# Kernel optimization log

Measured on AMD Instinct MI355X. Metric: run time of the kernel, lower is better.

The kernel has to match this reference:

```python
import jax, jax.numpy as jnp
import numpy as np

H, E, V, F, P, B = 512, 512, 10000, 1280, 196, 32
SOS = 1

def setup_inputs() -> dict:
    key = jax.random.key(0)
    ks = jax.random.split(key, 24)
    s = 0.02
    return {
        "feature_outputs": jax.random.normal(ks[0], (B, P, F), jnp.float32),
        "caption": jax.random.randint(ks[1], (B, 80), 0, V),
        "max_caption": 80,
        "embedding": jax.random.normal(ks[2], (V, E), jnp.float32) * s,
        "W1_w": jax.random.normal(ks[3], (H, H), jnp.float32) * s,
        "W1_b": jnp.full((H,), 0.01, jnp.float32),
        "W2_w": jax.random.normal(ks[4], (H, F), jnp.float32) * s,
        "W2_b": jnp.full((H,), 0.01, jnp.float32),
        "Va_w": jax.random.normal(ks[5], (1, H), jnp.float32) * s,
        "Va_b": jnp.full((1,), 0.01, jnp.float32),
        "lstm_Wih": jax.random.normal(ks[6], (4 * H, E + F), jnp.float32) * s,
        "lstm_Whh": jax.random.normal(ks[7], (4 * H, H), jnp.float32) * s,
        "lstm_bih": jnp.zeros((4 * H,), jnp.float32),
        "lstm_bhh": jnp.zeros((4 * H,), jnp.float32),
        "out_w": jax.random.normal(ks[8], (V, H), jnp.float32) * s,
        "out_b": jnp.full((V,), 0.01, jnp.float32),
        "init_h_w": jax.random.normal(ks[9], (H, F), jnp.float32) * s,
        "init_h_b": jnp.full((H,), 0.01, jnp.float32),
        "init_c_w": jax.random.normal(ks[10], (H, F), jnp.float32) * s,
        "init_c_b": jnp.full((H,), 0.01, jnp.float32),
        "gate_w": jax.random.normal(ks[11], (F, H), jnp.float32) * s,
        "gate_b": jnp.full((F,), 0.01, jnp.float32),
    }


def reference(feature_outputs, caption, max_caption, embedding,
              W1_w, W1_b, W2_w, W2_b, Va_w, Va_b,
              lstm_Wih, lstm_Whh, lstm_bih, lstm_bhh,
              out_w, out_b, init_h_w, init_h_b, init_c_w, init_c_b,
              gate_w, gate_b):
    steps = int(max_caption)
    bsz = caption.shape[0]
    mean_enc = feature_outputs.mean(axis=1)                       # [B,F]
    h0 = mean_enc @ init_h_w.T + init_h_b                         # [B,H]
    c0 = mean_enc @ init_c_w.T + init_c_b                         # [B,H]
    # W2(keys) is constant across steps -> hoist out of the loop
    enc_proj = jnp.einsum('bpf,hf->bph', feature_outputs, W2_w) + W2_b  # [B,P,H]
    inp0 = jnp.broadcast_to(embedding[SOS], (bsz, embedding.shape[1]))  # [B,E]

    def step(carry, _):
        h, c, inp = carry
        # Bahdanau attention
        hid = h @ W1_w.T + W1_b                                   # [B,H]
        scores = (jax.nn.relu(hid[:, None, :] + enc_proj) @ Va_w[0] + Va_b[0])  # [B,P]
        weights = jax.nn.softmax(scores, axis=1)
        context = jnp.einsum('bpf,bp->bf', feature_outputs, weights)  # [B,F]
        gate = jax.nn.sigmoid(h @ gate_w.T + gate_b)              # [B,F]
        context = context * gate
        # LSTMCell (torch gate order: i, f, g, o)
        x = jnp.concatenate([inp, context], axis=1)               # [B,E+F]
        gates = x @ lstm_Wih.T + lstm_bih + h @ lstm_Whh.T + lstm_bhh
        i_g, f_g, g_g, o_g = jnp.split(gates, 4, axis=1)
        c_new = jax.nn.sigmoid(f_g) * c + jax.nn.sigmoid(i_g) * jnp.tanh(g_g)
        h_new = jax.nn.sigmoid(o_g) * jnp.tanh(c_new)
        logits = h_new @ out_w.T + out_b                          # [B,V] (dropout = eval identity)
        nxt = embedding[jnp.argmax(logits, axis=-1)]              # greedy decode
        return (h_new, c_new, nxt), (logits, weights)

    (h, c, _), (outs, attns) = jax.lax.scan(step, (h0, c0, inp0), None, length=steps)
    decoder_outputs = jnp.transpose(outs, (1, 0, 2))              # [B,T,V]
    attentions = jnp.transpose(attns, (1, 0, 2))                  # [B,T,P]
    return decoder_outputs, (h, c), attentions
```

## Files before the change

kernel.cpp:

```cpp
#include <hip/hip_runtime.h>
#include <hip/hip_cooperative_groups.h>
#include <math.h>

#define RI __restrict__

namespace {

constexpr int Hn=512, En=512, Vn=10000, Fn=1280, Pn=196, Bn=32, Tn=80;
constexpr int G4 = 2048, KX = 1792;
constexpr int NCAT = 13888;
constexpr int NVT = 157;
constexpr int J_GATE = 512, J_XP = 1792, J_LOG = 3840;
constexpr int NBLK = 256;

constexpr long O_ENC  = 0;
constexpr long O_W2T  = O_ENC  + (long)Bn*Pn*Hn;
constexpr long O_WCAT = O_W2T  + (long)Fn*Hn;
constexpr long O_WIHT = O_WCAT + (long)Hn*NCAT;
constexpr long O_H    = O_WIHT + (long)KX*G4;
constexpr long O_HT   = O_H    + (long)Bn*Hn;
constexpr long O_C    = O_HT   + (long)Hn*Bn;
constexpr long O_HID  = O_C    + (long)Bn*Hn;
constexpr long O_GT   = O_HID  + (long)Bn*Hn;
constexpr long O_XPT  = O_GT   + (long)Bn*Fn;
constexpr long O_XT   = O_XPT  + (long)G4*Bn;
constexpr long O_PMV  = O_XT   + (long)Bn*KX;
constexpr long O_PMI  = O_PMV  + (long)Bn*NVT;
constexpr long O_SVAL = O_PMI  + (long)Bn*NVT;
constexpr long O_SEL  = O_SVAL + (long)Bn*Pn;
constexpr long O_CNT  = O_SEL  + 64;
constexpr long O_IHCT  = O_ENC;
constexpr long O_MEANT = O_ENC + (long)Fn*1024;

__device__ __forceinline__ float sigm(float x){ return 1.0f/(1.0f+expf(-x)); }
__device__ __forceinline__ void fma4(float4& a, const float4 x, const float w){
  a.x += w*x.x; a.y += w*x.y; a.z += w*x.z; a.w += w*x.w;
}
__device__ __forceinline__ float ldc(const float* p){
  return __hip_atomic_load(p, __ATOMIC_RELAXED, __HIP_MEMORY_SCOPE_AGENT);
}
__device__ __forceinline__ void stc(float* p, float v){
  __hip_atomic_store(p, v, __ATOMIC_RELAXED, __HIP_MEMORY_SCOPE_AGENT);
}
__device__ __forceinline__ int ldci(const int* p){
  return __hip_atomic_load(p, __ATOMIC_RELAXED, __HIP_MEMORY_SCOPE_AGENT);
}
__device__ __forceinline__ void stci(int* p, int v){
  __hip_atomic_store(p, v, __ATOMIC_RELAXED, __HIP_MEMORY_SCOPE_AGENT);
}
__device__ __forceinline__ float2 ldc2(const float* p){
  union { unsigned long long u; float2 f; } c;
  c.u = __hip_atomic_load((const unsigned long long*)p,
                          __ATOMIC_RELAXED, __HIP_MEMORY_SCOPE_AGENT);
  return c.f;
}

__device__ __forceinline__ void gbar(unsigned* cnt, unsigned target){
  __syncthreads();
  if (threadIdx.x == 0){
    __hip_atomic_fetch_add(cnt, 1u, __ATOMIC_RELAXED, __HIP_MEMORY_SCOPE_AGENT);
    while (__hip_atomic_load(cnt, __ATOMIC_RELAXED, __HIP_MEMORY_SCOPE_AGENT) < target)
      __builtin_amdgcn_s_sleep(2);
  }
  __syncthreads();
}

__global__ __launch_bounds__(256) void k_tr_s(const float* RI src, float* RI dst,
                                              int R, int C, int S){
  __shared__ float t[32][33];
  int tc0 = blockIdx.x*32, tr0 = blockIdx.y*32;
  int lx = threadIdx.x & 31, ly = threadIdx.x >> 5;
  for (int i = ly; i < 32; i += 8){
    int r = tr0 + i, c = tc0 + lx;
    t[i][lx] = (r < R && c < C) ? src[(long)r*C + c] : 0.f;
  }
  __syncthreads();
  for (int i = ly; i < 32; i += 8){
    int c = tc0 + i, r = tr0 + lx;
    if (c < C && r < R) dst[(long)c*S + r] = t[lx][i];
  }
}

__global__ __launch_bounds__(256) void k_tr_wih(const float* RI src, float* RI ws){
  __shared__ float t[32][33];
  int tk0 = blockIdx.x*32, tj0 = blockIdx.y*32;
  int lx = threadIdx.x & 31, ly = threadIdx.x >> 5;
  for (int i = ly; i < 32; i += 8){
    int j = tj0 + i, k = tk0 + lx;
    t[i][lx] = src[(long)j*KX + k];
  }
  __syncthreads();
  for (int i = ly; i < 32; i += 8){
    int k = tk0 + i, j = tj0 + lx;
    int pc = ((j & 511) << 2) | (j >> 9);
    ws[O_WIHT + (long)k*G4 + pc] = t[lx][i];
  }
}

__global__ __launch_bounds__(256) void k_mean(const float* RI feat, float* RI ws){
  int blk = blockIdx.x;
  int b = blk / 5, ft = blk % 5;
  int f = ft*256 + threadIdx.x;
  float s = 0.f;
  const float* fp = feat + (long)b*Pn*Fn + f;
  for (int p = 0; p < Pn; ++p) s += fp[(long)p*Fn];
  ws[O_MEANT + (long)f*Bn + b] = s * (1.0f/Pn);
}

__global__ __launch_bounds__(512) void k_h0c0(const float* RI ihb, const float* RI icb,
                                              float* RI ws){
  int tid = threadIdx.x;
  int jl = tid & 63, bq = tid >> 6;
  int j = blockIdx.x*64 + jl;
  const float* wp = ws + O_IHCT + j;
  const float* xp = ws + O_MEANT + bq*4;
  float4 acc = make_float4(0,0,0,0);
  for (int k = 0; k < Fn; ++k){
    float w = wp[(long)k*1024];
    float4 x = *(const float4*)(xp + (long)k*Bn);
    fma4(acc, x, w);
  }
  float va[4] = {acc.x, acc.y, acc.z, acc.w};
  if (j < Hn){
    float bias = ihb[j];
    #pragma unroll
    for (int m = 0; m < 4; ++m){
      int b = bq*4 + m;
      ws[O_HT + (long)j*Bn + b] = va[m] + bias;
    }
  } else {
    int j2 = j - Hn;
    float bias = icb[j2];
    #pragma unroll
    for (int m = 0; m < 4; ++m)
      ws[O_C + (long)(bq*4+m)*Hn + j2] = va[m] + bias;
  }
}

__global__ __launch_bounds__(512) void k_encproj(const float* RI feat, const float* RI w2b,
                                                 float* RI ws){
  __shared__ __align__(16) float xs[64*65];
  const int blk = blockIdx.x;
  const int rt = blk >> 2, ct = blk & 3;
  const int r0 = rt*64, j0 = ct*128;
  const int tid = threadIdx.x;
  const int jq = tid & 31, rg = tid >> 5;
  const int rw = tid >> 3, kc = (tid & 7)*8;
  const float* w2t = ws + O_W2T + j0 + jq*4;
  float4 a0 = make_float4(0,0,0,0), a1 = a0, a2 = a0, a3 = a0;
  for (int k0 = 0; k0 < Fn; k0 += 64){
    __syncthreads();
    {
      const float* fp = feat + (long)(r0+rw)*Fn + k0 + kc;
      float4 v0 = *(const float4*)(fp);
      float4 v1 = *(const float4*)(fp + 4);
      float* xr = xs + rw*65 + kc;
      xr[0]=v0.x; xr[1]=v0.y; xr[2]=v0.z; xr[3]=v0.w;
      xr[4]=v1.x; xr[5]=v1.y; xr[6]=v1.z; xr[7]=v1.w;
    }
    __syncthreads();
    #pragma unroll 4
    for (int kk = 0; kk < 64; ++kk){
      float4 w = *(const float4*)(w2t + (long)(k0+kk)*Hn);
      const float* xp = xs + (rg*4)*65 + kk;
      fma4(a0, w, xp[0]);
      fma4(a1, w, xp[65]);
      fma4(a2, w, xp[130]);
      fma4(a3, w, xp[195]);
    }
  }
  float4 b4 = *(const float4*)(w2b + j0 + jq*4);
  float4 out[4] = {a0,a1,a2,a3};
  #pragma unroll
  for (int m = 0; m < 4; ++m){
    long r = r0 + rg*4 + m;
    float4 o = out[m];
    o.x += b4.x; o.y += b4.y; o.z += b4.z; o.w += b4.w;
    *(float4*)(ws + O_ENC + r*Hn + j0 + jq*4) = o;
  }
}

__global__ __launch_bounds__(512) void k_decode(
    const float* RI feat, const float* RI emb, const float* RI vaw, const float* RI vab,
    const float* RI w1b, const float* RI gb, const float* RI bih, const float* RI bhh,
    const float* RI outb, float* RI ws, float* RI dout)
{
  __shared__ __align__(16) float wlds[32768];
  __shared__ __align__(16) float sbuf[4608];
  const int blk = blockIdx.x, tid = threadIdx.x;
  const int jl = tid & 63, bq = tid >> 6;
  unsigned* cnt = (unsigned*)(ws + O_CNT);

  if (blk < 217){
    const float* wg = ws + O_WCAT + blk*64;
    for (int idx = tid; idx < 512*64; idx += 512){
      int k = idx >> 6, j = idx & 63;
      wlds[idx] = wg[(long)k*NCAT + j];
    }
  }
  __syncthreads();

  for (int t = 0; t <= Tn; ++t){
    bool p1act;
    if (t == Tn)      p1act = (blk >= 60 && blk < 217);
    else if (t == 0)  p1act = (blk < 60);
    else              p1act = (blk < 217);
    if (p1act){
      float4 acc = make_float4(0,0,0,0);
      float2 pre0 = ldc2(ws + O_HT + tid*2);
      float2 pre1 = ldc2(ws + O_HT + 1024 + tid*2);
      for (int c8 = 0; c8 < 8; ++c8){
        __syncthreads();
        *(float2*)(sbuf + tid*2) = pre0;
        *(float2*)(sbuf + 1024 + tid*2) = pre1;
        __syncthreads();
        if (c8 < 7){
          pre0 = ldc2(ws + O_HT + (long)(c8+1)*2048 + tid*2);
          pre1 = ldc2(ws + O_HT + (long)(c8+1)*2048 + 1024 + tid*2);
        }
        #pragma unroll 8
        for (int kk = 0; kk < 64; ++kk){
          float w = wlds[(long)(c8*64 + kk)*64 + jl];
          float4 x = *(const float4*)(sbuf + kk*32 + bq*4);
          fma4(acc, x, w);
        }
      }
      __syncthreads();
      const int j = blk*64 + jl;
      if (blk < 8){
        float bias = w1b[j];
        stc(ws + O_HID + (long)(bq*4+0)*Hn + j, acc.x + bias);
        stc(ws + O_HID + (long)(bq*4+1)*Hn + j, acc.y + bias);
        stc(ws + O_HID + (long)(bq*4+2)*Hn + j, acc.z + bias);
        stc(ws + O_HID + (long)(bq*4+3)*Hn + j, acc.w + bias);
      } else if (blk < 28){
        int f = j - J_GATE;
        float bias = gb[f];
        stc(ws + O_GT + (long)(bq*4+0)*Fn + f, sigm(acc.x + bias));
        stc(ws + O_GT + (long)(bq*4+1)*Fn + f, sigm(acc.y + bias));
        stc(ws + O_GT + (long)(bq*4+2)*Fn + f, sigm(acc.z + bias));
        stc(ws + O_GT + (long)(bq*4+3)*Fn + f, sigm(acc.w + bias));
      } else if (blk < 60){
        int j2 = j - J_XP;
        float bias = bih[j2] + bhh[j2];
        sbuf[jl*33 + bq*4+0] = acc.x + bias;
        sbuf[jl*33 + bq*4+1] = acc.y + bias;
        sbuf[jl*33 + bq*4+2] = acc.z + bias;
        sbuf[jl*33 + bq*4+3] = acc.w + bias;
        __syncthreads();
        #pragma unroll
        for (int r = 0; r < 4; ++r){
          int idx = r*512 + tid;
          int row = idx >> 5, b = idx & 31;
          int j2r = (blk-28)*64 + row;
          int pc = ((j2r & 511) << 2) | (j2r >> 9);
          stc(ws + O_XPT + (long)pc*Bn + b, sbuf[row*33 + b]);
        }
      } else {
        int v = j - J_LOG;
        float lv[4];
        if (v < Vn){
          float bias = outb[v];
          lv[0]=acc.x+bias; lv[1]=acc.y+bias; lv[2]=acc.z+bias; lv[3]=acc.w+bias;
          #pragma unroll
          for (int m = 0; m < 4; ++m)
            dout[((long)(bq*4+m)*Tn + (t-1))*Vn + v] = lv[m];
        } else {
          lv[0]=lv[1]=lv[2]=lv[3]=-1e30f;
        }
        int tile = blk - 60;
        #pragma unroll
        for (int m = 0; m < 4; ++m){
          float bv = lv[m]; int bi = v;
          #pragma unroll
          for (int off = 32; off; off >>= 1){
            float ov = __shfl_down(bv, off, 64);
            int   oi = __shfl_down(bi, off, 64);
            if (ov > bv || (ov == bv && oi < bi)){ bv = ov; bi = oi; }
          }
          if (jl == 0){
            int b = bq*4 + m;
            stc (ws + O_PMV + (long)b*NVT + tile, bv);
            stci((int*)(ws + O_PMI) + (long)b*NVT + tile, bi);
          }
        }
      }
    }
    gbar(cnt, 256u*(t+1));
    if (t == Tn) break;

    if (blk < 224){
      const int b = blk & 31, part = blk >> 5;
      float* hid_s = sbuf;
      float* va_s  = sbuf + 512;
      float* sv    = sbuf + 1024;
      hid_s[tid] = ldc(ws + O_HID + (long)b*Hn + tid);
      va_s[tid]  = vaw[tid];
      __syncthreads();
      const int w = tid >> 6, l = tid & 63;
      const int p0 = part*28;
      const float* eb = ws + O_ENC + (long)b*Pn*Hn;
      for (int p = p0 + w; p < p0 + 28; p += 8){
        const float* er = eb + (long)p*Hn;
        float4 e0 = *(const float4*)(er + l*4);
        float4 e1 = *(const float4*)(er + 256 + l*4);
        float4 h0 = *(const float4*)(hid_s + l*4);
        float4 h1 = *(const float4*)(hid_s + 256 + l*4);
        float4 v0 = *(const float4*)(va_s + l*4);
        float4 v1 = *(const float4*)(va_s + 256 + l*4);
        float s = fmaxf(h0.x+e0.x,0.f)*v0.x + fmaxf(h0.y+e0.y,0.f)*v0.y
                + fmaxf(h0.z+e0.z,0.f)*v0.z + fmaxf(h0.w+e0.w,0.f)*v0.w
                + fmaxf(h1.x+e1.x,0.f)*v1.x + fmaxf(h1.y+e1.y,0.f)*v1.y
                + fmaxf(h1.z+e1.z,0.f)*v1.z + fmaxf(h1.w+e1.w,0.f)*v1.w;
        #pragma unroll
        for (int off = 32; off; off >>= 1) s += __shfl_down(s, off, 64);
        if (l == 0) sv[p - p0] = s + vab[0];
      }
      __syncthreads();
      if (tid < 28) stc(ws + O_SVAL + (long)b*Pn + p0 + tid, sv[tid]);
    } else {
      const int b = blk - 224;
      if (t == 0){
        if (tid == 0) stci((int*)(ws + O_SEL) + b, 1);
      } else if (tid < 64){
        float bv = -1e30f; int bi = 0x7fffffff;
        for (int q = tid; q < NVT; q += 64){
          float cv = ldc(ws + O_PMV + (long)b*NVT + q);
          if (cv > bv){ bv = cv; bi = ldci((const int*)(ws + O_PMI) + (long)b*NVT + q); }
        }
        #pragma unroll
        for (int off = 32; off; off >>= 1){
          float ov = __shfl_down(bv, off, 64);
          int   oi = __shfl_down(bi, off, 64);
          if (ov > bv || (ov == bv && oi < bi)){ bv = ov; bi = oi; }
        }
        if (tid == 0) stci((int*)(ws + O_SEL) + b, bi);
      }
    }
    gbar(cnt + 32, 256u*(t+1));

    {
      const int b = blk & 31, fr = blk >> 5;
      const int f0 = fr*160;
      float* svl = sbuf;
      float* wts = sbuf + 208;
      if (tid < Pn) svl[tid] = ldc(ws + O_SVAL + (long)b*Pn + tid);
      if (tid == 0) ((int*)sbuf)[450] = ldci((const int*)(ws + O_SEL) + b);
      __syncthreads();
      if (tid < 64){
        float m = -1e30f;
        for (int p = tid; p < Pn; p += 64) m = fmaxf(m, svl[p]);
        #pragma unroll
        for (int off = 32; off; off >>= 1) m = fmaxf(m, __shfl_xor(m, off, 64));
        float sm = 0.f;
        for (int p = tid; p < Pn; p += 64) sm += expf(svl[p] - m);
        #pragma unroll
        for (int off = 32; off; off >>= 1) sm += __shfl_xor(sm, off, 64);
        if (tid == 0){ sbuf[448] = m; sbuf[449] = 1.0f/sm; }
      }
      __syncthreads();
      if (tid < Pn){
        float wv = expf(svl[tid] - sbuf[448]) * sbuf[449];
        wts[tid] = wv;
        if (fr == 0)
          dout[(long)Bn*Tn*Vn + 2L*Bn*Hn + ((long)b*Tn + t)*Pn + tid] = wv;
      }
      __syncthreads();
      const int pp = tid / 160, fl = tid - pp*160;
      float a = 0.f;
      if (tid < 480){
        const int p0 = pp*66, pn = (pp == 2) ? 64 : 66;
        const float* fp = feat + ((long)b*Pn + p0)*Fn + f0 + fl;
        const float* wl = wts + p0;
        float a0=0.f, a1=0.f, a2=0.f, a3=0.f;
        int p = 0;
        for (; p + 4 <= pn; p += 4){
          a0 += wl[p+0] * fp[(long)(p+0)*Fn];
          a1 += wl[p+1] * fp[(long)(p+1)*Fn];
          a2 += wl[p+2] * fp[(long)(p+2)*Fn];
          a3 += wl[p+3] * fp[(long)(p+3)*Fn];
        }
        for (; p < pn; ++p) a0 += wl[p] * fp[(long)p*Fn];
        a = (a0 + a1) + (a2 + a3);
        if (pp > 0) sbuf[512 + (pp-1)*160 + fl] = a;
      }
      __syncthreads();
      if (tid < 160){
        float tot = a + sbuf[512 + tid] + sbuf[672 + tid];
        int f = f0 + tid;
        tot *= ldc(ws + O_GT + (long)b*Fn + f);
        stc(ws + O_XT + (long)b*KX + En + f, tot);
      }
      if (fr == 0){
        int row = ((int*)sbuf)[450];
        stc(ws + O_XT + (long)b*KX + tid, emb[(long)row*En + tid]);
      }
    }
    gbar(cnt + 64, 256u*(t+1));

    {
      const int c = tid & 7, ks = tid >> 3;
      const int pc0 = blk*8;
      const float* wg = ws + O_WIHT + pc0 + c;
      float4 acc4[8];
      #pragma unroll
      for (int q = 0; q < 8; ++q) acc4[q] = make_float4(0,0,0,0);
      float2 pre[4];
      #pragma unroll
      for (int r = 0; r < 4; ++r){
        int flat = r*1024 + tid*2;
        pre[r] = ldc2(ws + O_XT + (long)(flat >> 7)*KX + (flat & 127));
      }
      for (int ch = 0; ch < 14; ++ch){
        __syncthreads();
        #pragma unroll
        for (int r = 0; r < 4; ++r){
          int flat = r*1024 + tid*2;
          int kl = flat & 127, b = flat >> 7;
          sbuf[kl*36 + b]     = pre[r].x;
          sbuf[(kl+1)*36 + b] = pre[r].y;
        }
        __syncthreads();
        if (ch < 13){
          long k0n = (long)(ch+1)*128;
          #pragma unroll
          for (int r = 0; r < 4; ++r){
            int flat = r*1024 + tid*2;
            pre[r] = ldc2(ws + O_XT + (long)(flat >> 7)*KX + k0n + (flat & 127));
          }
        }
        const long kg0 = (long)ch*128;
        #pragma unroll
        for (int kk = 0; kk < 2; ++kk){
          int kl = ks*2 + kk;
          float w = wg[(kg0 + kl)*G4];
          const float* xb = sbuf + kl*36;
          #pragma unroll
          for (int q = 0; q < 8; ++q){
            float4 x = *(const float4*)(xb + q*4);
            fma4(acc4[q], x, w);
          }
        }
      }
      #pragma unroll
      for (int off = 8; off <= 32; off <<= 1){
        #pragma unroll
        for (int q = 0; q < 8; ++q){
          acc4[q].x += __shfl_xor(acc4[q].x, off, 64);
          acc4[q].y += __shfl_xor(acc4[q].y, off, 64);
          acc4[q].z += __shfl_xor(acc4[q].z, off, 64);
          acc4[q].w += __shfl_xor(acc4[q].w, off, 64);
        }
      }
      __syncthreads();
      const int wv = tid >> 6, lane = tid & 63;
      if (lane < 8){
        float* rb = sbuf + (wv*8 + lane)*32;
        #pragma unroll
        for (int q = 0; q < 8; ++q) *(float4*)(rb + q*4) = acc4[q];
      }
      __syncthreads();
      if (tid < 256){
        int cc = tid >> 5, b = tid & 31;
        float s = 0.f;
        #pragma unroll
        for (int w2 = 0; w2 < 8; ++w2) s += sbuf[(w2*8 + cc)*32 + b];
        s += ldc(ws + O_XPT + (long)(pc0 + cc)*Bn + b);
        sbuf[2048 + cc*32 + b] = s;
      }
      __syncthreads();
      if (tid < 64){
        int il = tid >> 5, b = tid & 31;
        int i = blk*2 + il;
        float gi  = sbuf[2048 + (il*4+0)*32 + b];
        float gf  = sbuf[2048 + (il*4+1)*32 + b];
        float gg2 = sbuf[2048 + (il*4+2)*32 + b];
        float go  = sbuf[2048 + (il*4+3)*32 + b];
        float c_ = ws[O_C + (long)b*Hn + i];
        float cn = sigm(gf)*c_ + sigm(gi)*tanhf(gg2);
        float hn = sigm(go)*tanhf(cn);
        ws[O_C + (long)b*Hn + i] = cn;
        stc(ws + O_HT + (long)i*Bn + b, hn);
        if (t == Tn-1){
          dout[(long)Bn*Tn*Vn + (long)b*Hn + i] = hn;
          dout[(long)Bn*Tn*Vn + (long)Bn*Hn + (long)b*Hn + i] = cn;
        }
      }
    }
    gbar(cnt + 96, 256u*(t+1));
  }
}

}

extern "C" void kernel_launch(void* const* d_in, const int* in_sizes, int n_in,
                              void* d_out, int out_size, void* d_ws, size_t ws_size,
                              hipStream_t stream)
{
  (void)in_sizes; (void)n_in; (void)out_size; (void)ws_size;
  const float* feat = (const float*)d_in[0];
  const float* emb  = (const float*)d_in[3];
  const float* w1w  = (const float*)d_in[4];
  const float* w1b  = (const float*)d_in[5];
  const float* w2w  = (const float*)d_in[6];
  const float* w2b  = (const float*)d_in[7];
  const float* vaw  = (const float*)d_in[8];
  const float* vab  = (const float*)d_in[9];
  const float* wih  = (const float*)d_in[10];
  const float* whh  = (const float*)d_in[11];
  const float* bih  = (const float*)d_in[12];
  const float* bhh  = (const float*)d_in[13];
  const float* outw = (const float*)d_in[14];
  const float* outb = (const float*)d_in[15];
  const float* ihw  = (const float*)d_in[16];
  const float* ihb  = (const float*)d_in[17];
  const float* icw  = (const float*)d_in[18];
  const float* icb  = (const float*)d_in[19];
  const float* gw   = (const float*)d_in[20];
  const float* gb   = (const float*)d_in[21];
  float* ws  = (float*)d_ws;
  float* out = (float*)d_out;

  hipMemsetAsync((char*)d_ws + O_CNT*sizeof(float), 0, 512, stream);

  k_tr_s<<<dim3(40,16),  256, 0, stream>>>(ihw,  ws + O_IHCT,       Hn, Fn, 1024);
  k_tr_s<<<dim3(40,16),  256, 0, stream>>>(icw,  ws + O_IHCT + 512, Hn, Fn, 1024);
  k_mean<<<160, 256, 0, stream>>>(feat, ws);
  k_h0c0<<<16, 512, 0, stream>>>(ihb, icb, ws);
  k_tr_s<<<dim3(16,16),  256, 0, stream>>>(w1w,  ws + O_WCAT,          Hn, Hn, NCAT);
  k_tr_s<<<dim3(16,40),  256, 0, stream>>>(gw,   ws + O_WCAT + J_GATE, Fn, Hn, NCAT);
  k_tr_s<<<dim3(16,64),  256, 0, stream>>>(whh,  ws + O_WCAT + J_XP,   G4, Hn, NCAT);
  k_tr_s<<<dim3(16,313), 256, 0, stream>>>(outw, ws + O_WCAT + J_LOG,  Vn, Hn, NCAT);
  k_tr_wih<<<dim3(56,64), 256, 0, stream>>>(wih, ws);
  k_tr_s<<<dim3(40,16),  256, 0, stream>>>(w2w,  ws + O_W2T,           Hn, Fn, Hn);
  k_encproj<<<392, 512, 0, stream>>>(feat, w2b, ws);

  void* kargs[] = { (void*)&feat, (void*)&emb, (void*)&vaw, (void*)&vab,
                    (void*)&w1b, (void*)&gb, (void*)&bih, (void*)&bhh,
                    (void*)&outb, (void*)&ws, (void*)&out };
  hipLaunchCooperativeKernel((const void*)k_decode, dim3(NBLK), dim3(512),
                             kargs, 0, stream);
}
```

Baseline: 6.517 ms.

## Use per-step ring slots for h/x and retile LSTM gate GEMM over 128 blocks

Hidden state and LSTM input vectors now go to per-timestep slots instead of one shared buffer. Readers can then use plain vectorised float4 loads rather than agent-scope atomic float2 loads, because no slot is overwritten while it is still being read. The Wih^T layout is repacked into 16-column panels, and the gate GEMM runs on 128 blocks with 16 gate columns each, using a padded LDS layout for x, double-buffered chunk prefetch and a shorter shuffle reduction. The context reduction also moves to 8 accumulators and the attention loop is unrolled. Half the blocks now sit idle in the gate phase, and the workspace grows to hold all time slots.

```diff
diff --git a/kernel.cpp b/kernel.cpp
--- a/kernel.cpp
+++ b/kernel.cpp
@@ -12,23 +12,25 @@
 constexpr int NVT = 157;
 constexpr int J_GATE = 512, J_XP = 1792, J_LOG = 3840;
 constexpr int NBLK = 256;
+constexpr int HTSL = 16448;
+constexpr int XTSL = 57408;
+constexpr int XROW = 140;
 
 constexpr long O_ENC  = 0;
 constexpr long O_W2T  = O_ENC  + (long)Bn*Pn*Hn;
 constexpr long O_WCAT = O_W2T  + (long)Fn*Hn;
 constexpr long O_WIHT = O_WCAT + (long)Hn*NCAT;
-constexpr long O_H    = O_WIHT + (long)KX*G4;
-constexpr long O_HT   = O_H    + (long)Bn*Hn;
-constexpr long O_C    = O_HT   + (long)Hn*Bn;
+constexpr long O_C    = O_WIHT + (long)KX*G4;
 constexpr long O_HID  = O_C    + (long)Bn*Hn;
 constexpr long O_GT   = O_HID  + (long)Bn*Hn;
 constexpr long O_XPT  = O_GT   + (long)Bn*Fn;
-constexpr long O_XT   = O_XPT  + (long)G4*Bn;
-constexpr long O_PMV  = O_XT   + (long)Bn*KX;
+constexpr long O_PMV  = O_XPT  + (long)G4*Bn;
 constexpr long O_PMI  = O_PMV  + (long)Bn*NVT;
 constexpr long O_SVAL = O_PMI  + (long)Bn*NVT;
 constexpr long O_SEL  = O_SVAL + (long)Bn*Pn;
 constexpr long O_CNT  = O_SEL  + 64;
+constexpr long O_HTR  = O_CNT  + 128;
+constexpr long O_XTR  = O_HTR  + 81L*HTSL;
 constexpr long O_IHCT  = O_ENC;
 constexpr long O_MEANT = O_ENC + (long)Fn*1024;
 
@@ -47,12 +49,6 @@
 }
 __device__ __forceinline__ void stci(int* p, int v){
   __hip_atomic_store(p, v, __ATOMIC_RELAXED, __HIP_MEMORY_SCOPE_AGENT);
-}
-__device__ __forceinline__ float2 ldc2(const float* p){
-  union { unsigned long long u; float2 f; } c;
-  c.u = __hip_atomic_load((const unsigned long long*)p,
-                          __ATOMIC_RELAXED, __HIP_MEMORY_SCOPE_AGENT);
-  return c.f;
 }
 
 __device__ __forceinline__ void gbar(unsigned* cnt, unsigned target){
@@ -93,7 +89,7 @@
   for (int i = ly; i < 32; i += 8){
     int k = tk0 + i, j = tj0 + lx;
     int pc = ((j & 511) << 2) | (j >> 9);
-    ws[O_WIHT + (long)k*G4 + pc] = t[lx][i];
+    ws[O_WIHT + ((long)(pc >> 4)*KX + k)*16 + (pc & 15)] = t[lx][i];
   }
 }
 
@@ -124,10 +120,8 @@
   if (j < Hn){
     float bias = ihb[j];
     #pragma unroll
-    for (int m = 0; m < 4; ++m){
-      int b = bq*4 + m;
-      ws[O_HT + (long)j*Bn + b] = va[m] + bias;
-    }
+    for (int m = 0; m < 4; ++m)
+      ws[O_HTR + (long)j*Bn + (bq*4+m)] = va[m] + bias;
   } else {
     int j2 = j - Hn;
     float bias = icb[j2];
@@ -206,18 +200,14 @@
     else if (t == 0)  p1act = (blk < 60);
     else              p1act = (blk < 217);
     if (p1act){
+      const float* htp = ws + O_HTR + (long)t*HTSL;
       float4 acc = make_float4(0,0,0,0);
-      float2 pre0 = ldc2(ws + O_HT + tid*2);
-      float2 pre1 = ldc2(ws + O_HT + 1024 + tid*2);
+      float4 pre = *(const float4*)(htp + tid*4);
       for (int c8 = 0; c8 < 8; ++c8){
         __syncthreads();
-        *(float2*)(sbuf + tid*2) = pre0;
-        *(float2*)(sbuf + 1024 + tid*2) = pre1;
-        __syncthreads();
-        if (c8 < 7){
-          pre0 = ldc2(ws + O_HT + (long)(c8+1)*2048 + tid*2);
-          pre1 = ldc2(ws + O_HT + (long)(c8+1)*2048 + 1024 + tid*2);
-        }
+        *(float4*)(sbuf + tid*4) = pre;
+        __syncthreads();
+        if (c8 < 7) pre = *(const float4*)(htp + (long)(c8+1)*2048 + tid*4);
         #pragma unroll 8
         for (int kk = 0; kk < 64; ++kk){
           float w = wlds[(long)(c8*64 + kk)*64 + jl];
@@ -300,6 +290,7 @@
       const int w = tid >> 6, l = tid & 63;
       const int p0 = part*28;
       const float* eb = ws + O_ENC + (long)b*Pn*Hn;
+      #pragma unroll 2
       for (int p = p0 + w; p < p0 + 28; p += 8){
         const float* er = eb + (long)p*Hn;
         float4 e0 = *(const float4*)(er + l*4);
@@ -342,6 +333,7 @@
     {
       const int b = blk & 31, fr = blk >> 5;
       const int f0 = fr*160;
+      float* xslot = ws + O_XTR + (long)t*XTSL;
       float* svl = sbuf;
       float* wts = sbuf + 208;
       if (tid < Pn) svl[tid] = ldc(ws + O_SVAL + (long)b*Pn + tid);
@@ -372,16 +364,20 @@
         const int p0 = pp*66, pn = (pp == 2) ? 64 : 66;
         const float* fp = feat + ((long)b*Pn + p0)*Fn + f0 + fl;
         const float* wl = wts + p0;
-        float a0=0.f, a1=0.f, a2=0.f, a3=0.f;
+        float s0=0,s1=0,s2=0,s3=0,s4=0,s5=0,s6=0,s7=0;
         int p = 0;
-        for (; p + 4 <= pn; p += 4){
-          a0 += wl[p+0] * fp[(long)(p+0)*Fn];
-          a1 += wl[p+1] * fp[(long)(p+1)*Fn];
-          a2 += wl[p+2] * fp[(long)(p+2)*Fn];
-          a3 += wl[p+3] * fp[(long)(p+3)*Fn];
-        }
-        for (; p < pn; ++p) a0 += wl[p] * fp[(long)p*Fn];
-        a = (a0 + a1) + (a2 + a3);
+        for (; p + 8 <= pn; p += 8){
+          s0 += wl[p+0]*fp[(long)(p+0)*Fn];
+          s1 += wl[p+1]*fp[(long)(p+1)*Fn];
+          s2 += wl[p+2]*fp[(long)(p+2)*Fn];
+          s3 += wl[p+3]*fp[(long)(p+3)*Fn];
+          s4 += wl[p+4]*fp[(long)(p+4)*Fn];
+          s5 += wl[p+5]*fp[(long)(p+5)*Fn];
+          s6 += wl[p+6]*fp[(long)(p+6)*Fn];
+          s7 += wl[p+7]*fp[(long)(p+7)*Fn];
+        }
+        for (; p < pn; ++p) s0 += wl[p]*fp[(long)p*Fn];
+        a = ((s0+s1)+(s2+s3)) + ((s4+s5)+(s6+s7));
         if (pp > 0) sbuf[512 + (pp-1)*160 + fl] = a;
       }
       __syncthreads();
@@ -389,61 +385,86 @@
         float tot = a + sbuf[512 + tid] + sbuf[672 + tid];
         int f = f0 + tid;
         tot *= ldc(ws + O_GT + (long)b*Fn + f);
-        stc(ws + O_XT + (long)b*KX + En + f, tot);
+        stc(xslot + (long)b*KX + En + f, tot);
       }
       if (fr == 0){
         int row = ((int*)sbuf)[450];
-        stc(ws + O_XT + (long)b*KX + tid, emb[(long)row*En + tid]);
+        stc(xslot + (long)b*KX + tid, emb[(long)row*En + tid]);
       }
     }
     gbar(cnt + 64, 256u*(t+1));
 
-    {
-      const int c = tid & 7, ks = tid >> 3;
-      const int pc0 = blk*8;
-      const float* wg = ws + O_WIHT + pc0 + c;
+    if (blk < 128){
+      const int c = tid & 15, ks = tid >> 4;
+      const int pc0 = blk*16;
+      const float* wg = ws + O_WIHT + (long)blk*KX*16;
+      const float* xrow = ws + O_XTR + (long)t*XTSL + (long)(tid >> 4)*KX;
+      const int skl = (tid & 15)*8;
+      const int sb = tid >> 4;
       float4 acc4[8];
       #pragma unroll
       for (int q = 0; q < 8; ++q) acc4[q] = make_float4(0,0,0,0);
-      float2 pre[4];
+      float4 pA0 = *(const float4*)(xrow + skl);
+      float4 pA1 = *(const float4*)(xrow + skl + 4);
+      float4 pB0 = *(const float4*)(xrow + 128 + skl);
+      float4 pB1 = *(const float4*)(xrow + 128 + skl + 4);
+      const int scs = skl + ((skl >> 5) << 2);
+      for (int ch = 0; ch < 14; ch += 2){
+        __syncthreads();
+        { float* xd = sbuf + sb*XROW;
+          *(float4*)(xd + scs) = pA0; *(float4*)(xd + scs + 4) = pA1; }
+        __syncthreads();
+        if (ch + 2 < 14){
+          pA0 = *(const float4*)(xrow + (long)(ch+2)*128 + skl);
+          pA1 = *(const float4*)(xrow + (long)(ch+2)*128 + skl + 4);
+        }
+        {
+          const long kg0 = (long)ch*128;
+          #pragma unroll
+          for (int kk = 0; kk < 4; ++kk){
+            int kl = ks + kk*32;
+            float w = wg[(kg0 + kl)*16 + c];
+            int cs = kl + ((kl >> 5) << 2);
+            const float* xq = sbuf + cs;
+            #pragma unroll
+            for (int q = 0; q < 8; ++q){
+              const float* xb = xq + (q*4)*XROW;
+              acc4[q].x += w * xb[0];
+              acc4[q].y += w * xb[XROW];
+              acc4[q].z += w * xb[2*XROW];
+              acc4[q].w += w * xb[3*XROW];
+            }
+          }
+        }
+        __syncthreads();
+        { float* xd = sbuf + sb*XROW;
+          *(float4*)(xd + scs) = pB0; *(float4*)(xd + scs + 4) = pB1; }
+        __syncthreads();
+        if (ch + 3 < 14){
+          pB0 = *(const float4*)(xrow + (long)(ch+3)*128 + skl);
+          pB1 = *(const float4*)(xrow + (long)(ch+3)*128 + skl + 4);
+        }
+        {
+          const long kg0 = (long)(ch+1)*128;
+          #pragma unroll
+          for (int kk = 0; kk < 4; ++kk){
+            int kl = ks + kk*32;
+            float w = wg[(kg0 + kl)*16 + c];
+            int cs = kl + ((kl >> 5) << 2);
+            const float* xq = sbuf + cs;
+            #pragma unroll
+            for (int q = 0; q < 8; ++q){
+              const float* xb = xq + (q*4)*XROW;
+              acc4[q].x += w * xb[0];
+              acc4[q].y += w * xb[XROW];
+              acc4[q].z += w * xb[2*XROW];
+              acc4[q].w += w * xb[3*XROW];
+            }
+          }
+        }
+      }
       #pragma unroll
-      for (int r = 0; r < 4; ++r){
-        int flat = r*1024 + tid*2;
-        pre[r] = ldc2(ws + O_XT + (long)(flat >> 7)*KX + (flat & 127));
-      }
-      for (int ch = 0; ch < 14; ++ch){
-        __syncthreads();
-        #pragma unroll
-        for (int r = 0; r < 4; ++r){
-          int flat = r*1024 + tid*2;
-          int kl = flat & 127, b = flat >> 7;
-          sbuf[kl*36 + b]     = pre[r].x;
-          sbuf[(kl+1)*36 + b] = pre[r].y;
-        }
-        __syncthreads();
-        if (ch < 13){
-          long k0n = (long)(ch+1)*128;
-          #pragma unroll
-          for (int r = 0; r < 4; ++r){
-            int flat = r*1024 + tid*2;
-            pre[r] = ldc2(ws + O_XT + (long)(flat >> 7)*KX + k0n + (flat & 127));
-          }
-        }
-        const long kg0 = (long)ch*128;
-        #pragma unroll
-        for (int kk = 0; kk < 2; ++kk){
-          int kl = ks*2 + kk;
-          float w = wg[(kg0 + kl)*G4];
-          const float* xb = sbuf + kl*36;
-          #pragma unroll
-          for (int q = 0; q < 8; ++q){
-            float4 x = *(const float4*)(xb + q*4);
-            fma4(acc4[q], x, w);
-          }
-        }
-      }
-      #pragma unroll
-      for (int off = 8; off <= 32; off <<= 1){
+      for (int off = 16; off <= 32; off <<= 1){
         #pragma unroll
         for (int q = 0; q < 8; ++q){
           acc4[q].x += __shfl_xor(acc4[q].x, off, 64);
@@ -454,33 +475,34 @@
       }
       __syncthreads();
       const int wv = tid >> 6, lane = tid & 63;
-      if (lane < 8){
-        float* rb = sbuf + (wv*8 + lane)*32;
+      if (lane < 16){
+        float* rb = sbuf + (wv*16 + lane)*32;
         #pragma unroll
         for (int q = 0; q < 8; ++q) *(float4*)(rb + q*4) = acc4[q];
       }
       __syncthreads();
-      if (tid < 256){
+      {
         int cc = tid >> 5, b = tid & 31;
         float s = 0.f;
         #pragma unroll
-        for (int w2 = 0; w2 < 8; ++w2) s += sbuf[(w2*8 + cc)*32 + b];
+        for (int w2 = 0; w2 < 8; ++w2) s += sbuf[(w2*16 + cc)*32 + b];
         s += ldc(ws + O_XPT + (long)(pc0 + cc)*Bn + b);
-        sbuf[2048 + cc*32 + b] = s;
-      }
-      __syncthreads();
-      if (tid < 64){
+        __syncthreads();
+        sbuf[4096 + cc*32 + b] = s;
+      }
+      __syncthreads();
+      if (tid < 128){
         int il = tid >> 5, b = tid & 31;
-        int i = blk*2 + il;
-        float gi  = sbuf[2048 + (il*4+0)*32 + b];
-        float gf  = sbuf[2048 + (il*4+1)*32 + b];
-        float gg2 = sbuf[2048 + (il*4+2)*32 + b];
-        float go  = sbuf[2048 + (il*4+3)*32 + b];
+        int i = blk*4 + il;
+        float gi  = sbuf[4096 + (il*4+0)*32 + b];
+        float gf  = sbuf[4096 + (il*4+1)*32 + b];
+        float gg2 = sbuf[4096 + (il*4+2)*32 + b];
+        float go  = sbuf[4096 + (il*4+3)*32 + b];
         float c_ = ws[O_C + (long)b*Hn + i];
         float cn = sigm(gf)*c_ + sigm(gi)*tanhf(gg2);
         float hn = sigm(go)*tanhf(cn);
         ws[O_C + (long)b*Hn + i] = cn;
-        stc(ws + O_HT + (long)i*Bn + b, hn);
+        stc(ws + O_HTR + (long)(t+1)*HTSL + (long)i*Bn + b, hn);
         if (t == Tn-1){
           dout[(long)Bn*Tn*Vn + (long)b*Hn + i] = hn;
           dout[(long)Bn*Tn*Vn + (long)Bn*Hn + (long)b*Hn + i] = cn;
```

Result: slower. 8.534 ms (+30.9%).

## Block W_ih^T by column group and re-layout shared x tile

Applied to the files above, without the earlier changes.

Rearranges the transposed LSTM input weights so that each block's 8 gate columns sit together over all K. Per-block weight reads become contiguous instead of strided by 2048. The shared-memory staging of x switches to a batch-major layout with padded rows, which changes how x is read in the inner loop from float4 loads to scalar strided loads. The change also widens the attention context reduction to 8 accumulators with nontemporal loads of the features, and unrolls the score loop by 2. The scalar shared-memory reads may add LDS instruction count, and the new row padding may or may not avoid bank conflicts.

```diff
diff --git a/kernel.cpp b/kernel.cpp
--- a/kernel.cpp
+++ b/kernel.cpp
@@ -12,15 +12,15 @@
 constexpr int NVT = 157;
 constexpr int J_GATE = 512, J_XP = 1792, J_LOG = 3840;
 constexpr int NBLK = 256;
+constexpr int XROW = 140;
 
 constexpr long O_ENC  = 0;
 constexpr long O_W2T  = O_ENC  + (long)Bn*Pn*Hn;
 constexpr long O_WCAT = O_W2T  + (long)Fn*Hn;
 constexpr long O_WIHT = O_WCAT + (long)Hn*NCAT;
-constexpr long O_H    = O_WIHT + (long)KX*G4;
-constexpr long O_HT   = O_H    + (long)Bn*Hn;
-constexpr long O_C    = O_HT   + (long)Hn*Bn;
-constexpr long O_HID  = O_C    + (long)Bn*Hn;
+constexpr long O_C    = O_WIHT + (long)KX*G4;
+constexpr long O_HT   = O_C    + (long)Bn*Hn;
+constexpr long O_HID  = O_HT   + (long)Hn*Bn;
 constexpr long O_GT   = O_HID  + (long)Bn*Hn;
 constexpr long O_XPT  = O_GT   + (long)Bn*Fn;
 constexpr long O_XT   = O_XPT  + (long)G4*Bn;
@@ -93,7 +93,7 @@
   for (int i = ly; i < 32; i += 8){
     int k = tk0 + i, j = tj0 + lx;
     int pc = ((j & 511) << 2) | (j >> 9);
-    ws[O_WIHT + (long)k*G4 + pc] = t[lx][i];
+    ws[O_WIHT + ((long)(pc >> 3)*KX + k)*8 + (pc & 7)] = t[lx][i];
   }
 }
 
@@ -124,10 +124,8 @@
   if (j < Hn){
     float bias = ihb[j];
     #pragma unroll
-    for (int m = 0; m < 4; ++m){
-      int b = bq*4 + m;
-      ws[O_HT + (long)j*Bn + b] = va[m] + bias;
-    }
+    for (int m = 0; m < 4; ++m)
+      ws[O_HT + (long)j*Bn + (bq*4+m)] = va[m] + bias;
   } else {
     int j2 = j - Hn;
     float bias = icb[j2];
@@ -300,6 +298,7 @@
       const int w = tid >> 6, l = tid & 63;
       const int p0 = part*28;
       const float* eb = ws + O_ENC + (long)b*Pn*Hn;
+      #pragma unroll 2
       for (int p = p0 + w; p < p0 + 28; p += 8){
         const float* er = eb + (long)p*Hn;
         float4 e0 = *(const float4*)(er + l*4);
@@ -372,16 +371,20 @@
         const int p0 = pp*66, pn = (pp == 2) ? 64 : 66;
         const float* fp = feat + ((long)b*Pn + p0)*Fn + f0 + fl;
         const float* wl = wts + p0;
-        float a0=0.f, a1=0.f, a2=0.f, a3=0.f;
+        float s0=0,s1=0,s2=0,s3=0,s4=0,s5=0,s6=0,s7=0;
         int p = 0;
-        for (; p + 4 <= pn; p += 4){
-          a0 += wl[p+0] * fp[(long)(p+0)*Fn];
-          a1 += wl[p+1] * fp[(long)(p+1)*Fn];
-          a2 += wl[p+2] * fp[(long)(p+2)*Fn];
-          a3 += wl[p+3] * fp[(long)(p+3)*Fn];
-        }
-        for (; p < pn; ++p) a0 += wl[p] * fp[(long)p*Fn];
-        a = (a0 + a1) + (a2 + a3);
+        for (; p + 8 <= pn; p += 8){
+          s0 += wl[p+0]*__builtin_nontemporal_load(fp + (long)(p+0)*Fn);
+          s1 += wl[p+1]*__builtin_nontemporal_load(fp + (long)(p+1)*Fn);
+          s2 += wl[p+2]*__builtin_nontemporal_load(fp + (long)(p+2)*Fn);
+          s3 += wl[p+3]*__builtin_nontemporal_load(fp + (long)(p+3)*Fn);
+          s4 += wl[p+4]*__builtin_nontemporal_load(fp + (long)(p+4)*Fn);
+          s5 += wl[p+5]*__builtin_nontemporal_load(fp + (long)(p+5)*Fn);
+          s6 += wl[p+6]*__builtin_nontemporal_load(fp + (long)(p+6)*Fn);
+          s7 += wl[p+7]*__builtin_nontemporal_load(fp + (long)(p+7)*Fn);
+        }
+        for (; p < pn; ++p) s0 += wl[p]*__builtin_nontemporal_load(fp + (long)p*Fn);
+        a = ((s0+s1)+(s2+s3)) + ((s4+s5)+(s6+s7));
         if (pp > 0) sbuf[512 + (pp-1)*160 + fl] = a;
       }
       __syncthreads();
@@ -401,7 +404,7 @@
     {
       const int c = tid & 7, ks = tid >> 3;
       const int pc0 = blk*8;
-      const float* wg = ws + O_WIHT + pc0 + c;
+      const float* wg = ws + O_WIHT + (long)blk*KX*8;
       float4 acc4[8];
       #pragma unroll
       for (int q = 0; q < 8; ++q) acc4[q] = make_float4(0,0,0,0);
@@ -417,8 +420,9 @@
         for (int r = 0; r < 4; ++r){
           int flat = r*1024 + tid*2;
           int kl = flat & 127, b = flat >> 7;
-          sbuf[kl*36 + b]     = pre[r].x;
-          sbuf[(kl+1)*36 + b] = pre[r].y;
+          int sc = kl + ((kl >> 5) << 2);
+          float* xd = sbuf + b*XROW;
+          xd[sc] = pre[r].x; xd[sc+1] = pre[r].y;
         }
         __syncthreads();
         if (ch < 13){
@@ -433,12 +437,16 @@
         #pragma unroll
         for (int kk = 0; kk < 2; ++kk){
           int kl = ks*2 + kk;
-          float w = wg[(kg0 + kl)*G4];
-          const float* xb = sbuf + kl*36;
+          float w = wg[(kg0 + kl)*8 + c];
+          int cs = kl + ((kl >> 5) << 2);
+          const float* xq = sbuf + cs;
           #pragma unroll
           for (int q = 0; q < 8; ++q){
-            float4 x = *(const float4*)(xb + q*4);
-            fma4(acc4[q], x, w);
+            const float* xb = xq + (q*4)*XROW;
+            acc4[q].x += w * xb[0];
+            acc4[q].y += w * xb[XROW];
+            acc4[q].z += w * xb[2*XROW];
+            acc4[q].w += w * xb[3*XROW];
           }
         }
       }
```

Result: no change. 6.401 ms (-1.8%).
